# Kernel optimization log

Measured on AMD Instinct MI355X. Metric: run time of the kernel, lower is better.

Reference implementation:

```python
import jax, jax.numpy as jnp
import numpy as np

N = 5
B = 1048576
RANGE = jnp.asarray([np.pi / 2, np.pi, np.pi / 2, np.pi, np.pi / 2], dtype=jnp.float32)
NUM_STEPS = 10


def setup_inputs() -> dict:
    key = jax.random.key(0)
    ks = jax.random.split(key, 9)
    return {
        "obs": jax.random.normal(ks[0], (B, 10), dtype=jnp.float32),
        "t": jax.random.uniform(ks[1], (B,), dtype=jnp.float32) * 10.0,
        "dt": jnp.full((1,), 0.01, dtype=jnp.float32),
        "mu_p": jax.random.normal(ks[2], (N,), dtype=jnp.float32),
        "a": jax.random.normal(ks[3], (N,), dtype=jnp.float32),
        "w": jax.random.normal(ks[4], (N, N), dtype=jnp.float32),
        "phi": jax.random.normal(ks[5], (N, N), dtype=jnp.float32),
        "frequencies": jax.random.normal(ks[6], (N,), dtype=jnp.float32),
        "amplitudes": jax.random.normal(ks[7], (N,), dtype=jnp.float32),
        "phases": jax.random.normal(ks[8], (N,), dtype=jnp.float32),
        "std": jnp.ones((N,), dtype=jnp.float32) * 0.5,
    }


def _dynamics(r, r_dot, theta, mu_p, a, w, phi, frequencies):
    # r, r_dot, theta: [b, N]
    r_dot_dot = a * (a / 4 * (mu_p - r) - r_dot)
    # diff[b,i,j] = theta_j - theta_i - phi_ij
    diff = theta[:, None, :] - theta[:, :, None] - phi[None, :, :]
    coupling = jnp.einsum("ij,bij,bj->bi", w, jnp.sin(diff), r)
    theta_dot = frequencies[None, :] + coupling
    return r_dot_dot, theta_dot


def _rk4_step(r, r_dot, theta, dt, mu_p, a, w, phi, frequencies):
    rdd1, td1 = _dynamics(r, r_dot, theta, mu_p, a, w, phi, frequencies)
    k1_r, k1_rd, k1_t = r_dot, rdd1, td1
    rdd2, td2 = _dynamics(r + 0.5 * dt * k1_r, r_dot + 0.5 * dt * k1_rd, theta + 0.5 * dt * k1_t,
                          mu_p, a, w, phi, frequencies)
    k2_r, k2_rd, k2_t = r_dot + 0.5 * dt * k1_rd, rdd2, td2
    rdd3, td3 = _dynamics(r + 0.5 * dt * k2_r, r_dot + 0.5 * dt * k2_rd, theta + 0.5 * dt * k2_t,
                          mu_p, a, w, phi, frequencies)
    k3_r, k3_rd, k3_t = r_dot + 0.5 * dt * k2_rd, rdd3, td3
    rdd4, td4 = _dynamics(r + dt * k3_r, r_dot + dt * k3_rd, theta + dt * k3_t,
                          mu_p, a, w, phi, frequencies)
    k4_r, k4_rd, k4_t = r_dot + dt * k3_rd, rdd4, td4
    r = r + dt / 6 * (k1_r + 2 * k2_r + 2 * k3_r + k4_r)
    r_dot = r_dot + dt / 6 * (k1_rd + 2 * k2_rd + 2 * k3_rd + k4_rd)
    theta = theta + dt / 6 * (k1_t + 2 * k2_t + 2 * k3_t + k4_t)
    return r, r_dot, theta


def reference(obs, t, dt, mu_p, a, w, phi, frequencies, amplitudes, phases, std):
    b = t.shape[0]
    dt_s = dt[0]
    r = jnp.zeros((b, N), dtype=t.dtype)
    r_dot = jnp.zeros_like(r)
    theta = jnp.zeros_like(r)

    def body(_, carry):
        r, r_dot, theta = carry
        return _rk4_step(r, r_dot, theta, dt_s, mu_p, a, w, phi, frequencies)

    r, r_dot, theta = jax.lax.fori_loop(0, NUM_STEPS, body, (r, r_dot, theta))

    f = jax.nn.softplus(frequencies)                 # true frequencies
    amp = jnp.tanh(amplitudes) * RANGE               # true amplitudes
    p = jax.nn.softplus(phases)                      # true phases
    two_pi = jnp.float32(2.0 * np.pi)
    mu = amp[None, :] * jnp.sin(two_pi * f[None, :] * t[:, None] + p[None, :])  # [b, N]
    std_full = jnp.ones_like(mu) * std[None, :]
    # stack distribution params + live CPG state: [4, b, N]
    return jnp.stack([mu, std_full, r, theta], axis=0)
```

## Files before the change

### kernel.cpp

```cpp
#include <hip/hip_runtime.h>
#include <math.h>

constexpr int kN      = 5;
constexpr int kB      = 1048576;
constexpr int kBN     = kB * kN;
constexpr int kBN4    = kBN / 4;
constexpr int kSteps  = 10;
constexpr int kBlocks = 1280;
constexpr int kThreads = 256;
constexpr unsigned kStride  = kBlocks * kThreads;
constexpr int      kIters   = kBN4 / kStride;
constexpr unsigned kStrideB = 4u * kStride / 5u;

static_assert(kStride % 5u == 0, "grid stride must be 0 mod 5 for loop-invariant phase");
static_assert(kIters * kStride == (unsigned)kBN4, "exact coverage, no bounds check needed");

typedef float floatx4 __attribute__((ext_vector_type(4)));

__device__ __forceinline__ void cpg_dynamics(float r, float rd, float th,
                                             float mu, float a,
                                             const float wr[kN], const float ph[kN],
                                             float freq, float& rdd, float& thd)
{
    rdd = a * (a * 0.25f * (mu - r) - rd);
    float coup = 0.f;
#pragma unroll
    for (int j = 0; j < kN; ++j) {
        float th_j = __shfl(th, j);
        float r_j  = __shfl(r, j);
        coup = __builtin_fmaf(wr[j] * __sinf(th_j - th - ph[j]), r_j, coup);
    }
    thd = freq + coup;
}

__device__ __forceinline__ float softplus_f(float x)
{
    return fmaxf(x, 0.f) + log1pf(expf(-fabsf(x)));
}

__global__ __launch_bounds__(kThreads)
void ijspeert_kernel(const float* __restrict__ t,
                     const float* __restrict__ dt_p,
                     const float* __restrict__ mu_p,
                     const float* __restrict__ a_p,
                     const float* __restrict__ w_p,
                     const float* __restrict__ phi_p,
                     const float* __restrict__ freq_p,
                     const float* __restrict__ amp_p,
                     const float* __restrict__ phase_p,
                     const float* __restrict__ std_p,
                     float* __restrict__ out)
{
    __shared__ float s_amp[kN], s_w2[kN], s_p[kN], s_std[kN], s_r[kN], s_th[kN];

    if (threadIdx.x < 64) {
        const int i = (threadIdx.x < kN) ? (int)threadIdx.x : 0;
        const float dt = dt_p[0];
        const float mu = mu_p[i];
        const float a  = a_p[i];
        const float fr = freq_p[i];
        float wr[kN], ph[kN];
#pragma unroll
        for (int j = 0; j < kN; ++j) {
            wr[j] = w_p[i * kN + j];
            ph[j] = phi_p[i * kN + j];
        }

        float r = 0.f, rd = 0.f, th = 0.f;
        for (int s = 0; s < kSteps; ++s) {
            float rdd1, td1, rdd2, td2, rdd3, td3, rdd4, td4;
            cpg_dynamics(r, rd, th, mu, a, wr, ph, fr, rdd1, td1);
            const float k1_r = rd, k1_rd = rdd1, k1_t = td1;
            cpg_dynamics(r + 0.5f * dt * k1_r, rd + 0.5f * dt * k1_rd,
                         th + 0.5f * dt * k1_t, mu, a, wr, ph, fr, rdd2, td2);
            const float k2_r = rd + 0.5f * dt * k1_rd, k2_rd = rdd2, k2_t = td2;
            cpg_dynamics(r + 0.5f * dt * k2_r, rd + 0.5f * dt * k2_rd,
                         th + 0.5f * dt * k2_t, mu, a, wr, ph, fr, rdd3, td3);
            const float k3_r = rd + 0.5f * dt * k2_rd, k3_rd = rdd3, k3_t = td3;
            cpg_dynamics(r + dt * k3_r, rd + dt * k3_rd,
                         th + dt * k3_t, mu, a, wr, ph, fr, rdd4, td4);
            const float k4_r = rd + dt * k3_rd, k4_rd = rdd4, k4_t = td4;
            const float c = dt * (1.f / 6.f);
            r  += c * (k1_r  + 2.f * k2_r  + 2.f * k3_r  + k4_r);
            rd += c * (k1_rd + 2.f * k2_rd + 2.f * k3_rd + k4_rd);
            th += c * (k1_t  + 2.f * k2_t  + 2.f * k3_t  + k4_t);
        }

        if (threadIdx.x < kN) {
            const float pi  = 3.14159265358979323846f;
            const float rng = (i & 1) ? pi : (0.5f * pi);
            const float f_true = softplus_f(fr);
            s_w2[i]  = 2.f * pi * f_true;
            s_amp[i] = tanhf(amp_p[i]) * rng;
            s_p[i]   = softplus_f(phase_p[i]);
            s_std[i] = std_p[i];
            s_r[i]   = r;
            s_th[i]  = th;
        }
    }
    __syncthreads();

    const unsigned gid = blockIdx.x * kThreads + threadIdx.x;
    const unsigned m   = (4u * gid) % 5u;
    unsigned b = (4u * gid - m) / 5u;
    unsigned q = gid;

    float ampk[4], w2k[4], pk[4];
    floatx4 vs, vr4, vt4;
#pragma unroll
    for (int k = 0; k < 4; ++k) {
        unsigned ik = m + (unsigned)k;
        if (ik >= 5u) ik -= 5u;
        ampk[k] = s_amp[ik];
        w2k[k]  = s_w2[ik];
        pk[k]   = s_p[ik];
        vs[k]   = s_std[ik];
        vr4[k]  = s_r[ik];
        vt4[k]  = s_th[ik];
    }

    floatx4* o = reinterpret_cast<floatx4*>(out);

#pragma unroll
    for (int it = 0; it < kIters; ++it) {
        const float t0 = t[b];
        const unsigned b1 = (b + 1u < (unsigned)kB) ? (b + 1u) : (unsigned)(kB - 1);
        const float t1 = t[b1];

        floatx4 vm;
#pragma unroll
        for (int k = 0; k < 4; ++k) {
            const float tb = ((m + (unsigned)k) >= 5u) ? t1 : t0;
            vm[k] = ampk[k] * __sinf(__builtin_fmaf(w2k[k], tb, pk[k]));
        }

        __builtin_nontemporal_store(vm,  &o[q]);
        __builtin_nontemporal_store(vs,  &o[kBN4 + q]);
        __builtin_nontemporal_store(vr4, &o[2 * kBN4 + q]);
        __builtin_nontemporal_store(vt4, &o[3 * kBN4 + q]);

        q += kStride;
        b += kStrideB;
    }
}

extern "C" void kernel_launch(void* const* d_in, const int* in_sizes, int n_in,
                              void* d_out, int out_size, void* d_ws, size_t ws_size,
                              hipStream_t stream)
{
    const float* t      = (const float*)d_in[1];
    const float* dt     = (const float*)d_in[2];
    const float* mu_p   = (const float*)d_in[3];
    const float* a      = (const float*)d_in[4];
    const float* w      = (const float*)d_in[5];
    const float* phi    = (const float*)d_in[6];
    const float* freq   = (const float*)d_in[7];
    const float* amp    = (const float*)d_in[8];
    const float* phase  = (const float*)d_in[9];
    const float* stdv   = (const float*)d_in[10];
    float* out = (float*)d_out;

    ijspeert_kernel<<<kBlocks, kThreads, 0, stream>>>(
        t, dt, mu_p, a, w, phi, freq, amp, phase, stdv, out);
}
```

Baseline: 139.1 us.

## Split output planes across dedicated block groups to specialize work per block

Blocks are now partitioned into four groups, each writing one output plane (mu, std, r, theta). Only the r/theta blocks run the serial RK4 integration prologue, and only mu blocks read t and evaluate sin, so std blocks skip the CPG computation entirely. The aim is to shorten the per-block serial prologue for half the grid and give each block a simpler store stream. In exchange, the mu blocks carry all the transcendental work, which can leave the load unbalanced across the grid.

```diff
diff --git a/kernel.cpp b/kernel.cpp
--- a/kernel.cpp
+++ b/kernel.cpp
@@ -6,14 +6,16 @@
 constexpr int kBN     = kB * kN;
 constexpr int kBN4    = kBN / 4;
 constexpr int kSteps  = 10;
-constexpr int kBlocks = 1280;
 constexpr int kThreads = 256;
-constexpr unsigned kStride  = kBlocks * kThreads;
-constexpr int      kIters   = kBN4 / kStride;
-constexpr unsigned kStrideB = 4u * kStride / 5u;
 
-static_assert(kStride % 5u == 0, "grid stride must be 0 mod 5 for loop-invariant phase");
-static_assert(kIters * kStride == (unsigned)kBN4, "exact coverage, no bounds check needed");
+constexpr int kBlocksPerPlane = 320;
+constexpr int kBlocksTotal    = 4 * kBlocksPerPlane;
+constexpr unsigned kPlaneThreads = kBlocksPerPlane * kThreads;
+constexpr int      kItersPP      = kBN4 / kPlaneThreads;
+constexpr unsigned kStrideB      = 4u * kPlaneThreads / 5u;
+
+static_assert((4u * kPlaneThreads) % 5u == 0, "phase must be loop-invariant");
+static_assert(kItersPP * kPlaneThreads == (unsigned)kBN4, "exact coverage");
 
 typedef float floatx4 __attribute__((ext_vector_type(4)));
 
@@ -51,96 +53,105 @@
                      const float* __restrict__ std_p,
                      float* __restrict__ out)
 {
-    __shared__ float s_amp[kN], s_w2[kN], s_p[kN], s_std[kN], s_r[kN], s_th[kN];
+    const int plane = blockIdx.x / kBlocksPerPlane;
+    const int pblk  = blockIdx.x % kBlocksPerPlane;
+    const unsigned ql = (unsigned)pblk * kThreads + threadIdx.x;
 
-    if (threadIdx.x < 64) {
-        const int i = (threadIdx.x < kN) ? (int)threadIdx.x : 0;
-        const float dt = dt_p[0];
-        const float mu = mu_p[i];
-        const float a  = a_p[i];
-        const float fr = freq_p[i];
-        float wr[kN], ph[kN];
-#pragma unroll
-        for (int j = 0; j < kN; ++j) {
-            wr[j] = w_p[i * kN + j];
-            ph[j] = phi_p[i * kN + j];
-        }
+    const unsigned m = (4u * ql) % 5u;
+    unsigned b = (4u * ql - m) / 5u;
+    unsigned q = ql;
 
-        float r = 0.f, rd = 0.f, th = 0.f;
-        for (int s = 0; s < kSteps; ++s) {
-            float rdd1, td1, rdd2, td2, rdd3, td3, rdd4, td4;
-            cpg_dynamics(r, rd, th, mu, a, wr, ph, fr, rdd1, td1);
-            const float k1_r = rd, k1_rd = rdd1, k1_t = td1;
-            cpg_dynamics(r + 0.5f * dt * k1_r, rd + 0.5f * dt * k1_rd,
-                         th + 0.5f * dt * k1_t, mu, a, wr, ph, fr, rdd2, td2);
-            const float k2_r = rd + 0.5f * dt * k1_rd, k2_rd = rdd2, k2_t = td2;
-            cpg_dynamics(r + 0.5f * dt * k2_r, rd + 0.5f * dt * k2_rd,
-                         th + 0.5f * dt * k2_t, mu, a, wr, ph, fr, rdd3, td3);
-            const float k3_r = rd + 0.5f * dt * k2_rd, k3_rd = rdd3, k3_t = td3;
-            cpg_dynamics(r + dt * k3_r, rd + dt * k3_rd,
-                         th + dt * k3_t, mu, a, wr, ph, fr, rdd4, td4);
-            const float k4_r = rd + dt * k3_rd, k4_rd = rdd4, k4_t = td4;
-            const float c = dt * (1.f / 6.f);
-            r  += c * (k1_r  + 2.f * k2_r  + 2.f * k3_r  + k4_r);
-            rd += c * (k1_rd + 2.f * k2_rd + 2.f * k3_rd + k4_rd);
-            th += c * (k1_t  + 2.f * k2_t  + 2.f * k3_t  + k4_t);
-        }
-
-        if (threadIdx.x < kN) {
-            const float pi  = 3.14159265358979323846f;
-            const float rng = (i & 1) ? pi : (0.5f * pi);
-            const float f_true = softplus_f(fr);
-            s_w2[i]  = 2.f * pi * f_true;
-            s_amp[i] = tanhf(amp_p[i]) * rng;
-            s_p[i]   = softplus_f(phase_p[i]);
-            s_std[i] = std_p[i];
-            s_r[i]   = r;
-            s_th[i]  = th;
-        }
-    }
-    __syncthreads();
-
-    const unsigned gid = blockIdx.x * kThreads + threadIdx.x;
-    const unsigned m   = (4u * gid) % 5u;
-    unsigned b = (4u * gid - m) / 5u;
-    unsigned q = gid;
-
-    float ampk[4], w2k[4], pk[4];
-    floatx4 vs, vr4, vt4;
+    unsigned ik[4];
 #pragma unroll
     for (int k = 0; k < 4; ++k) {
-        unsigned ik = m + (unsigned)k;
-        if (ik >= 5u) ik -= 5u;
-        ampk[k] = s_amp[ik];
-        w2k[k]  = s_w2[ik];
-        pk[k]   = s_p[ik];
-        vs[k]   = s_std[ik];
-        vr4[k]  = s_r[ik];
-        vt4[k]  = s_th[ik];
+        unsigned v = m + (unsigned)k;
+        ik[k] = (v >= 5u) ? (v - 5u) : v;
     }
 
-    floatx4* o = reinterpret_cast<floatx4*>(out);
+    floatx4* o = reinterpret_cast<floatx4*>(out) + (size_t)plane * kBN4;
 
-#pragma unroll
-    for (int it = 0; it < kIters; ++it) {
-        const float t0 = t[b];
-        const unsigned b1 = (b + 1u < (unsigned)kB) ? (b + 1u) : (unsigned)(kB - 1);
-        const float t1 = t[b1];
-
-        floatx4 vm;
+    if (plane == 0) {
+        const float pi = 3.14159265358979323846f;
+        float ampk[4], w2k[4], pk[4];
 #pragma unroll
         for (int k = 0; k < 4; ++k) {
-            const float tb = ((m + (unsigned)k) >= 5u) ? t1 : t0;
-            vm[k] = ampk[k] * __sinf(__builtin_fmaf(w2k[k], tb, pk[k]));
+            const unsigned i = ik[k];
+            const float rng = (i & 1u) ? pi : (0.5f * pi);
+            ampk[k] = tanhf(amp_p[i]) * rng;
+            w2k[k]  = 2.f * pi * softplus_f(freq_p[i]);
+            pk[k]   = softplus_f(phase_p[i]);
         }
+#pragma unroll
+        for (int it = 0; it < kItersPP; ++it) {
+            const float t0 = t[b];
+            const unsigned b1 = (b + 1u < (unsigned)kB) ? (b + 1u) : (unsigned)(kB - 1);
+            const float t1 = t[b1];
+            floatx4 vm;
+#pragma unroll
+            for (int k = 0; k < 4; ++k) {
+                const float tb = ((m + (unsigned)k) >= 5u) ? t1 : t0;
+                vm[k] = ampk[k] * __sinf(__builtin_fmaf(w2k[k], tb, pk[k]));
+            }
+            __builtin_nontemporal_store(vm, &o[q]);
+            q += kPlaneThreads;
+            b += kStrideB;
+        }
+    } else if (plane == 1) {
+        floatx4 vs;
+#pragma unroll
+        for (int k = 0; k < 4; ++k) vs[k] = std_p[ik[k]];
+#pragma unroll
+        for (int it = 0; it < kItersPP; ++it) {
+            __builtin_nontemporal_store(vs, &o[q]);
+            q += kPlaneThreads;
+        }
+    } else {
+        __shared__ float s_r[kN], s_th[kN];
+        if (threadIdx.x < 64) {
+            const int i = (threadIdx.x < kN) ? (int)threadIdx.x : 0;
+            const float dt = dt_p[0];
+            const float mu = mu_p[i];
+            const float a  = a_p[i];
+            const float fr = freq_p[i];
+            float wr[kN], ph[kN];
+#pragma unroll
+            for (int j = 0; j < kN; ++j) {
+                wr[j] = w_p[i * kN + j];
+                ph[j] = phi_p[i * kN + j];
+            }
 
-        __builtin_nontemporal_store(vm,  &o[q]);
-        __builtin_nontemporal_store(vs,  &o[kBN4 + q]);
-        __builtin_nontemporal_store(vr4, &o[2 * kBN4 + q]);
-        __builtin_nontemporal_store(vt4, &o[3 * kBN4 + q]);
+            float r = 0.f, rd = 0.f, th = 0.f;
+            for (int s = 0; s < kSteps; ++s) {
+                float rdd1, td1, rdd2, td2, rdd3, td3, rdd4, td4;
+                cpg_dynamics(r, rd, th, mu, a, wr, ph, fr, rdd1, td1);
+                const float k1_r = rd, k1_rd = rdd1, k1_t = td1;
+                cpg_dynamics(r + 0.5f * dt * k1_r, rd + 0.5f * dt * k1_rd,
+                             th + 0.5f * dt * k1_t, mu, a, wr, ph, fr, rdd2, td2);
+                const float k2_r = rd + 0.5f * dt * k1_rd, k2_rd = rdd2, k2_t = td2;
+                cpg_dynamics(r + 0.5f * dt * k2_r, rd + 0.5f * dt * k2_rd,
+                             th + 0.5f * dt * k2_t, mu, a, wr, ph, fr, rdd3, td3);
+                const float k3_r = rd + 0.5f * dt * k2_rd, k3_rd = rdd3, k3_t = td3;
+                cpg_dynamics(r + dt * k3_r, rd + dt * k3_rd,
+                             th + dt * k3_t, mu, a, wr, ph, fr, rdd4, td4);
+                const float k4_r = rd + dt * k3_rd, k4_rd = rdd4, k4_t = td4;
+                const float c = dt * (1.f / 6.f);
+                r  += c * (k1_r  + 2.f * k2_r  + 2.f * k3_r  + k4_r);
+                rd += c * (k1_rd + 2.f * k2_rd + 2.f * k3_rd + k4_rd);
+                th += c * (k1_t  + 2.f * k2_t  + 2.f * k3_t  + k4_t);
+            }
+            if (threadIdx.x < kN) { s_r[i] = r; s_th[i] = th; }
+        }
+        __syncthreads();
 
-        q += kStride;
-        b += kStrideB;
+        const float* src = (plane == 2) ? s_r : s_th;
+        floatx4 v;
+#pragma unroll
+        for (int k = 0; k < 4; ++k) v[k] = src[ik[k]];
+#pragma unroll
+        for (int it = 0; it < kItersPP; ++it) {
+            __builtin_nontemporal_store(v, &o[q]);
+            q += kPlaneThreads;
+        }
     }
 }
 
@@ -160,6 +171,6 @@
     const float* stdv   = (const float*)d_in[10];
     float* out = (float*)d_out;
 
-    ijspeert_kernel<<<kBlocks, kThreads, 0, stream>>>(
+    ijspeert_kernel<<<kBlocksTotal, kThreads, 0, stream>>>(
         t, dt, mu_p, a, w, phi, freq, amp, phase, stdv, out);
 }
```

Result: faster. 131.5 us (-5.5%).
